# Kernel optimization log

Measured on AMD Instinct MI355X. Metric: run time of the kernel, lower is better.

Reference implementation:

```python
import jax, jax.numpy as jnp
from jax import lax
import numpy as np

B, N_VARS, M_CLAUSES, K_DIM = 1024, 64, 256, 12
MAX_ITER = 12


def setup_inputs() -> dict:
    key = jax.random.key(0)
    k1, k2, k3, k4 = jax.random.split(key, 4)
    z = jax.random.uniform(k1, (B, N_VARS), dtype=jnp.float32)          # input probabilities
    S = jax.random.normal(k2, (M_CLAUSES, N_VARS + 1), dtype=jnp.float32) * 0.2  # learnable clause matrix (col 0 = truth var)
    w = jax.random.uniform(k3, (M_CLAUSES,), dtype=jnp.float32)          # learnable clause weights
    r = jax.random.normal(k4, (B, N_VARS, K_DIM), dtype=jnp.float32)     # random init directions
    return {"z": z, "S": S, "w": w, "r": r, "max_iter": MAX_ITER}


def _mixing(z, S, w, r, max_iter):
    Bsz, n = z.shape
    m, N = S.shape  # N = n + 1 (truth variable is column 0)
    k = r.shape[-1]
    eps = jnp.float32(1e-8)

    # truth direction v_T = e_0
    vT = jnp.zeros((k,), dtype=z.dtype).at[0].set(1.0)

    # random unit directions orthogonal to v_T (zero out component along e_0)
    r_perp = r.at[..., 0].set(0.0)
    r_perp = r_perp / jnp.maximum(jnp.linalg.norm(r_perp, axis=-1, keepdims=True), eps)

    # SATNet init: v_i = -cos(pi z_i) v_T + sin(pi z_i) r_perp_i
    ang = jnp.pi * z
    Vvars = -jnp.cos(ang)[..., None] * vT + jnp.sin(ang)[..., None] * r_perp  # [B,n,k]
    V = jnp.concatenate([jnp.broadcast_to(vT, (Bsz, 1, k)), Vvars], axis=1)   # [B,N,k]

    Sw = S * w[:, None]                       # weighted clause matrix [m,N]
    W = jnp.einsum('mn,bnk->bmk', Sw, V)      # running product Sw @ V, [B,m,k]
    snrm = jnp.sum(Sw * Sw, axis=0)           # ||s_i||^2 per variable, [N]

    def coord_step(carry, i):
        V, W = carry
        s_i = Sw[:, i]                         # [m]
        v_old = V[:, i, :]                     # [B,k]
        g = jnp.einsum('bmk,m->bk', W, s_i) - snrm[i] * v_old
        v_new = -g / jnp.maximum(jnp.linalg.norm(g, axis=-1, keepdims=True), eps)
        W = W + (v_new - v_old)[:, None, :] * s_i[None, :, None]  # rank-1 update
        V = V.at[:, i, :].set(v_new)
        return (V, W), None

    def sweep(carry, _):
        carry, _ = lax.scan(coord_step, carry, jnp.arange(1, N))  # coordinate descent over variables
        return carry, None

    (V, _), _ = lax.scan(sweep, (V, W), None, length=max_iter)

    # output probabilities: z_i = arccos(-v_i . v_T) / pi
    cos = jnp.clip(-V[:, 1:, 0], -1.0 + 1e-6, 1.0 - 1e-6)
    return jnp.arccos(cos) / jnp.pi


def reference(z, S, w, r, max_iter):
    return _mixing(z, S, w, r, max_iter)
```

## Files before the change

kernel.cpp:

```cpp
#include <hip/hip_runtime.h>
#include <math.h>

#define BATCH 1024
#define NV    64
#define MC    256
#define KD    12
#define PI_F  3.14159265358979323846f

#define CBUF   4544
#define C0OFF  4352
#define DGAOFF 4416
#define DGBOFF 4480

template <int CTRL>
__device__ __forceinline__ float dpp_addf(float x) {
  int y = __builtin_amdgcn_update_dpp(0, __float_as_int(x), CTRL, 0xF, 0xF, true);
  return x + __int_as_float(y);
}
__device__ __forceinline__ float allreduce16(float x) {
  x = dpp_addf<0xB1>(x);
  x = dpp_addf<0x4E>(x);
  x = dpp_addf<0x124>(x);
  x = dpp_addf<0x128>(x);
  return x;
}
__device__ __forceinline__ float readlane63(float x) {
  return __int_as_float(__builtin_amdgcn_readlane(__float_as_int(x), 63));
}

__global__ void compute_C_kernel(const float* __restrict__ S,
                                 const float* __restrict__ w,
                                 float* __restrict__ Cg, int nsplit) {
  const int q = blockIdx.x;
  const int mc = blockIdx.y;
  const int j = threadIdx.x;
  if (j > NV) return;
  const int v = (q + 1) % 64 + 1;
  const int mlen = MC / nsplit;
  const int m0 = mc * mlen;
  float a0 = 0.f, a1 = 0.f, a2 = 0.f, a3 = 0.f;
  for (int m = m0; m < m0 + mlen; m += 4) {
    const float w0 = w[m], w1 = w[m + 1], w2 = w[m + 2], w3 = w[m + 3];
    a0 = fmaf(S[(m + 0) * (NV + 1) + v] * w0 * w0, S[(m + 0) * (NV + 1) + j], a0);
    a1 = fmaf(S[(m + 1) * (NV + 1) + v] * w1 * w1, S[(m + 1) * (NV + 1) + j], a1);
    a2 = fmaf(S[(m + 2) * (NV + 1) + v] * w2 * w2, S[(m + 2) * (NV + 1) + j], a2);
    a3 = fmaf(S[(m + 3) * (NV + 1) + v] * w3 * w3, S[(m + 3) * (NV + 1) + j], a3);
  }
  const float acc = (a0 + a1) + (a2 + a3);
  float* buf = Cg + mc * CBUF;
  if (j == 0) buf[C0OFF + q] = acc;
  else        buf[q * 68 + (j - 1)] = acc;
  const int p1 = (v == 1) ? 64 : (v - 1);
  const int p2 = (v == 1) ? 63 : (v == 2) ? 64 : (v - 2);
  if (j == p1) buf[DGAOFF + (v - 1)] = acc;
  if (j == p2) buf[DGBOFF + (v - 1)] = acc;
}

__global__ __launch_bounds__(256, 1) void mixing_kernel(
    const float* __restrict__ z, const float* __restrict__ r,
    const float* __restrict__ Cg, const int* __restrict__ max_iter_p,
    float* __restrict__ out, int nsplit) {
  __shared__ float Ls[CBUF];

  const int t = threadIdx.x;
  const int l = t & 63;
  const int kq = l >> 4;
  const int n16 = l & 15;
  const int b = blockIdx.x * 4 + (t >> 6);
  const int max_iter = max_iter_p[0];

  {
    const float4* src = (const float4*)Cg;
    float4* dst = (float4*)Ls;
    for (int idx = t; idx < CBUF / 4; idx += 256) {
      float4 a = src[idx];
      for (int u = 1; u < nsplit; ++u) {
        const float4 p = src[u * (CBUF / 4) + idx];
        a.x += p.x; a.y += p.y; a.z += p.z; a.w += p.w;
      }
      dst[idx] = a;
    }
  }

  const float row0 = (kq == 0) ? 1.f : 0.f;

  float V[4][3];
  #pragma unroll
  for (int s = 0; s < 4; ++s) {
    const int n = 4 * n16 + s;
    const float zv = z[b * NV + n];
    float rp[3];
    float ssp = 0.f;
    #pragma unroll
    for (int j = 0; j < 3; ++j) {
      const int k = 3 * kq + j;
      rp[j] = (k == 0) ? 0.f : r[(b * NV + n) * KD + k];
      ssp = fmaf(rp[j], rp[j], ssp);
    }
    ssp += __shfl_xor(ssp, 16, 64);
    ssp += __shfl_xor(ssp, 32, 64);
    const float inv = 1.f / fmaxf(sqrtf(ssp), 1e-8f);
    float sn, cs;
    sincosf(PI_F * zv, &sn, &cs);
    #pragma unroll
    for (int j = 0; j < 3; ++j) {
      const int k = 3 * kq + j;
      V[s][j] = (k == 0) ? -cs : sn * rp[j] * inv;
    }
  }

  __syncthreads();

  const float4* C4   = (const float4*)Ls;
  const float4* C04  = (const float4*)(Ls + C0OFF);
  const float4* DgA4 = (const float4*)(Ls + DGAOFF);
  const float4* DgB4 = (const float4*)(Ls + DGBOFF);

  float P[3], vp1[3], vp2[3];

  {
    float4 ce = C4[63 * 17 + n16];
    const float c0 = Ls[C0OFF + 63];
    const bool l15 = (n16 == 15), l0 = (n16 == 0);
    ce.z = l15 ? 0.f : ce.z;
    ce.w = l15 ? 0.f : ce.w;
    ce.x = l0 ? 0.f : ce.x;
    float q0 = ce.x * V[0][0];
    float q1 = ce.x * V[0][1];
    float q2 = ce.x * V[0][2];
    q0 = fmaf(ce.y, V[1][0], q0); q1 = fmaf(ce.y, V[1][1], q1); q2 = fmaf(ce.y, V[1][2], q2);
    q0 = fmaf(ce.z, V[2][0], q0); q1 = fmaf(ce.z, V[2][1], q1); q2 = fmaf(ce.z, V[2][2], q2);
    q0 = fmaf(ce.w, V[3][0], q0); q1 = fmaf(ce.w, V[3][1], q1); q2 = fmaf(ce.w, V[3][2], q2);
    q0 = allreduce16(q0);
    q1 = allreduce16(q1);
    q2 = allreduce16(q2);
    q0 = fmaf(row0, c0, q0);
    P[0] = q0; P[1] = q1; P[2] = q2;
    const int src = l | 15;
    #pragma unroll
    for (int j = 0; j < 3; ++j) {
      vp1[j] = __shfl(V[3][j], src, 64);
      vp2[j] = __shfl(V[2][j], src, 64);
    }
  }

  float4 cbA[4], cbB[4], c0A, c0B, daA, daB, dbA, dbB;

  auto prefetch = [&](float4 cb[4], float4& c0b, float4& dab, float4& dbb, int g) {
    #pragma unroll
    for (int s = 0; s < 4; ++s) cb[s] = C4[(4 * g + s) * 17 + n16];
    c0b = C04[g];
    dab = DgA4[g];
    dbb = DgB4[g];
  };

  auto do_group = [&](int ii, const float4 cb[4], const float4& c0b,
                      const float4& dab, const float4& dbb) {
    const bool own  = (n16 == ii);
    const bool ownP = (n16 == ((ii + 15) & 15));
    const bool ownN = (n16 == ((ii + 1) & 15));
    const float* c0p = &c0b.x;
    const float* dap = &dab.x;
    const float* dbp = &dbb.x;
    #pragma unroll
    for (int s = 0; s < 4; ++s) {
      float4 ce = cb[s];
      if (s == 0) { ce.w = ownP ? 0.f : ce.w; ce.x = own ? 0.f : ce.x; ce.y = own ? 0.f : ce.y; }
      if (s == 1) { ce.x = own ? 0.f : ce.x;  ce.y = own ? 0.f : ce.y; ce.z = own ? 0.f : ce.z; }
      if (s == 2) { ce.y = own ? 0.f : ce.y;  ce.z = own ? 0.f : ce.z; ce.w = own ? 0.f : ce.w; }
      if (s == 3) { ce.z = own ? 0.f : ce.z;  ce.w = own ? 0.f : ce.w; ce.x = ownN ? 0.f : ce.x; }
      float q0 = ce.x * V[0][0];
      float q1 = ce.x * V[0][1];
      float q2 = ce.x * V[0][2];
      q0 = fmaf(ce.y, V[1][0], q0); q1 = fmaf(ce.y, V[1][1], q1); q2 = fmaf(ce.y, V[1][2], q2);
      q0 = fmaf(ce.z, V[2][0], q0); q1 = fmaf(ce.z, V[2][1], q1); q2 = fmaf(ce.z, V[2][2], q2);
      q0 = fmaf(ce.w, V[3][0], q0); q1 = fmaf(ce.w, V[3][1], q1); q2 = fmaf(ce.w, V[3][2], q2);
      q0 = allreduce16(q0);
      q1 = allreduce16(q1);
      q2 = allreduce16(q2);
      q0 = fmaf(row0, c0p[s], q0);

      float g0 = fmaf(dbp[s], vp2[0], P[0]);
      float g1 = fmaf(dbp[s], vp2[1], P[1]);
      float g2 = fmaf(dbp[s], vp2[2], P[2]);
      g0 = fmaf(dap[s], vp1[0], g0);
      g1 = fmaf(dap[s], vp1[1], g1);
      g2 = fmaf(dap[s], vp1[2], g2);
      const float t0 = g0 * g0, t1 = g1 * g1, t2 = g2 * g2;
      float n2p = (t0 + t1) + t2;
      n2p = dpp_addf<0x142>(n2p);
      n2p = dpp_addf<0x143>(n2p);
      const float n2 = readlane63(n2p);
      const float inv = __builtin_amdgcn_rsqf(fmaxf(n2, 1e-16f));
      const float v0 = -g0 * inv, v1 = -g1 * inv, v2 = -g2 * inv;

      if (s == 0) {
        V[3][0] = ownP ? vp1[0] : V[3][0];
        V[3][1] = ownP ? vp1[1] : V[3][1];
        V[3][2] = ownP ? vp1[2] : V[3][2];
      } else {
        V[s - 1][0] = own ? vp1[0] : V[s - 1][0];
        V[s - 1][1] = own ? vp1[1] : V[s - 1][1];
        V[s - 1][2] = own ? vp1[2] : V[s - 1][2];
      }

      vp2[0] = vp1[0]; vp2[1] = vp1[1]; vp2[2] = vp1[2];
      vp1[0] = v0;     vp1[1] = v1;     vp1[2] = v2;
      P[0] = q0; P[1] = q1; P[2] = q2;
    }
  };

  prefetch(cbA, c0A, daA, dbA, 0);

  for (int it = 0; it < max_iter; ++it) {
    for (int ih = 0; ih < 8; ++ih) {
      prefetch(cbB, c0B, daB, dbB, 2 * ih + 1);
      do_group(2 * ih, cbA, c0A, daA, dbA);
      prefetch(cbA, c0A, daA, dbA, (2 * ih + 2) & 15);
      do_group(2 * ih + 1, cbB, c0B, daB, dbB);
    }
  }

  {
    const bool l15 = (n16 == 15);
    V[3][0] = l15 ? vp1[0] : V[3][0];
    V[3][1] = l15 ? vp1[1] : V[3][1];
    V[3][2] = l15 ? vp1[2] : V[3][2];
  }

  if (kq == 0) {
    float4 o;
    float* op = &o.x;
    #pragma unroll
    for (int s = 0; s < 4; ++s) {
      float cv = -V[s][0];
      cv = fminf(fmaxf(cv, -1.f + 1e-6f), 1.f - 1e-6f);
      op[s] = acosf(cv) * (1.f / PI_F);
    }
    ((float4*)(out + b * NV))[n16] = o;
  }
}

extern "C" void kernel_launch(void* const* d_in, const int* in_sizes, int n_in,
                              void* d_out, int out_size, void* d_ws, size_t ws_size,
                              hipStream_t stream) {
  const float* z = (const float*)d_in[0];
  const float* S = (const float*)d_in[1];
  const float* w = (const float*)d_in[2];
  const float* r = (const float*)d_in[3];
  const int* max_iter = (const int*)d_in[4];
  float* Cg = (float*)d_ws;

  const int nsplit = (ws_size >= (size_t)4 * CBUF * 4) ? 4 : 1;
  compute_C_kernel<<<dim3(NV, nsplit), 128, 0, stream>>>(S, w, Cg, nsplit);
  mixing_kernel<<<BATCH / 4, 256, 0, stream>>>(z, r, Cg, max_iter,
                                               (float*)d_out, nsplit);
}
```

Measured before the change: 158.9 us.

## Pre-zero masked coupling entries, add convergence early exit, and split C wider

Zeroes the diagonal and neighbour coupling entries once in the precompute kernel, so the per-step lane masking selects in the mixing loop can go. Adds a per-wavefront early exit that stops the sweeps once no V component changes by more than 1e-6. Also fuses the squared-norm sum into FMAs and splits the C precompute across up to eight clause chunks when workspace allows. The early exit can cut iterations short relative to the fixed max_iter in the reference, which risks small numerical differences, and it adds snapshot registers plus a ballot per sweep.

After: 153.9 us. -3.2%, faster.

```diff
diff --git a/kernel.cpp b/kernel.cpp
--- a/kernel.cpp
+++ b/kernel.cpp
@@ -48,12 +48,15 @@
   }
   const float acc = (a0 + a1) + (a2 + a3);
   float* buf = Cg + mc * CBUF;
-  if (j == 0) buf[C0OFF + q] = acc;
-  else        buf[q * 68 + (j - 1)] = acc;
   const int p1 = (v == 1) ? 64 : (v - 1);
   const int p2 = (v == 1) ? 63 : (v == 2) ? 64 : (v - 2);
+  if (j == 0) buf[C0OFF + q] = acc;
   if (j == p1) buf[DGAOFF + (v - 1)] = acc;
   if (j == p2) buf[DGBOFF + (v - 1)] = acc;
+  if (j > 0) {
+    const float st = (j == v || j == p1 || j == p2) ? 0.f : acc;
+    buf[q * 68 + (j - 1)] = st;
+  }
 }
 
 __global__ __launch_bounds__(256, 1) void mixing_kernel(
@@ -119,12 +122,8 @@
   float P[3], vp1[3], vp2[3];
 
   {
-    float4 ce = C4[63 * 17 + n16];
+    const float4 ce = C4[63 * 17 + n16];
     const float c0 = Ls[C0OFF + 63];
-    const bool l15 = (n16 == 15), l0 = (n16 == 0);
-    ce.z = l15 ? 0.f : ce.z;
-    ce.w = l15 ? 0.f : ce.w;
-    ce.x = l0 ? 0.f : ce.x;
     float q0 = ce.x * V[0][0];
     float q1 = ce.x * V[0][1];
     float q2 = ce.x * V[0][2];
@@ -158,17 +157,12 @@
                       const float4& dab, const float4& dbb) {
     const bool own  = (n16 == ii);
     const bool ownP = (n16 == ((ii + 15) & 15));
-    const bool ownN = (n16 == ((ii + 1) & 15));
     const float* c0p = &c0b.x;
     const float* dap = &dab.x;
     const float* dbp = &dbb.x;
     #pragma unroll
     for (int s = 0; s < 4; ++s) {
-      float4 ce = cb[s];
-      if (s == 0) { ce.w = ownP ? 0.f : ce.w; ce.x = own ? 0.f : ce.x; ce.y = own ? 0.f : ce.y; }
-      if (s == 1) { ce.x = own ? 0.f : ce.x;  ce.y = own ? 0.f : ce.y; ce.z = own ? 0.f : ce.z; }
-      if (s == 2) { ce.y = own ? 0.f : ce.y;  ce.z = own ? 0.f : ce.z; ce.w = own ? 0.f : ce.w; }
-      if (s == 3) { ce.z = own ? 0.f : ce.z;  ce.w = own ? 0.f : ce.w; ce.x = ownN ? 0.f : ce.x; }
+      const float4 ce = cb[s];
       float q0 = ce.x * V[0][0];
       float q1 = ce.x * V[0][1];
       float q2 = ce.x * V[0][2];
@@ -186,8 +180,9 @@
       g0 = fmaf(dap[s], vp1[0], g0);
       g1 = fmaf(dap[s], vp1[1], g1);
       g2 = fmaf(dap[s], vp1[2], g2);
-      const float t0 = g0 * g0, t1 = g1 * g1, t2 = g2 * g2;
-      float n2p = (t0 + t1) + t2;
+      float n2p = g0 * g0;
+      n2p = fmaf(g1, g1, n2p);
+      n2p = fmaf(g2, g2, n2p);
       n2p = dpp_addf<0x142>(n2p);
       n2p = dpp_addf<0x143>(n2p);
       const float n2 = readlane63(n2p);
@@ -213,12 +208,25 @@
   prefetch(cbA, c0A, daA, dbA, 0);
 
   for (int it = 0; it < max_iter; ++it) {
+    float Vs[4][3];
+    #pragma unroll
+    for (int s = 0; s < 4; ++s) {
+      Vs[s][0] = V[s][0]; Vs[s][1] = V[s][1]; Vs[s][2] = V[s][2];
+    }
     for (int ih = 0; ih < 8; ++ih) {
       prefetch(cbB, c0B, daB, dbB, 2 * ih + 1);
       do_group(2 * ih, cbA, c0A, daA, dbA);
       prefetch(cbA, c0A, daA, dbA, (2 * ih + 2) & 15);
       do_group(2 * ih + 1, cbB, c0B, daB, dbB);
     }
+    float d = 0.f;
+    #pragma unroll
+    for (int s = 0; s < 4; ++s) {
+      d = fmaxf(d, fabsf(V[s][0] - Vs[s][0]));
+      d = fmaxf(d, fabsf(V[s][1] - Vs[s][1]));
+      d = fmaxf(d, fabsf(V[s][2] - Vs[s][2]));
+    }
+    if (__ballot(d > 1e-6f) == 0ull) break;
   }
 
   {
@@ -251,7 +259,8 @@
   const int* max_iter = (const int*)d_in[4];
   float* Cg = (float*)d_ws;
 
-  const int nsplit = (ws_size >= (size_t)4 * CBUF * 4) ? 4 : 1;
+  const int nsplit = (ws_size >= (size_t)8 * CBUF * 4) ? 8
+                   : (ws_size >= (size_t)4 * CBUF * 4) ? 4 : 1;
   compute_C_kernel<<<dim3(NV, nsplit), 128, 0, stream>>>(S, w, Cg, nsplit);
   mixing_kernel<<<BATCH / 4, 256, 0, stream>>>(z, r, Cg, max_iter,
                                                (float*)d_out, nsplit);
```
